# Kernel tuning notes

Hardware: AMD Instinct MI355X
Metric: run time of the kernel (lower is better)

Reference implementation:

```python
import jax, jax.numpy as jnp
import numpy as np

SCALE = 2  # scale_factor (isotropic Vec3i broadcast of init arg)
N_VOXELS = 262144
CHANNELS = 64


def setup_inputs() -> dict:
    key = jax.random.key(0)
    k1, k2 = jax.random.split(key)
    coarse_data = jax.random.normal(k1, (N_VOXELS, CHANNELS), dtype=jnp.float32)
    coarse_ijk = jax.random.randint(k2, (N_VOXELS, 3), 0, 512, dtype=jnp.int32)
    return {"coarse_data": coarse_data, "coarse_ijk": coarse_ijk}


def reference(coarse_data, coarse_ijk):
    """Nearest-neighbor subdivision of a sparse voxel grid.

    Each coarse voxel (ijk, feature) expands into SCALE**3 fine voxels at
    ijk*SCALE + offset, all carrying the parent's feature (nearest upsampling).
    Returns (fine_data [N*s^3, C], fine_ijk [N*s^3, 3]).
    """
    s = SCALE
    n_sub = s * s * s
    # offsets within each subdivided cell: [s^3, 3]
    offsets = jnp.stack(jnp.meshgrid(jnp.arange(s), jnp.arange(s), jnp.arange(s),
                                     indexing="ij"), axis=-1).reshape(-1, 3).astype(coarse_ijk.dtype)
    # fine coordinates: [N, s^3, 3] -> [N*s^3, 3]
    fine_ijk = (coarse_ijk[:, None, :] * s + offsets[None, :, :]).reshape(-1, 3)
    # nearest upsampling: repeat each coarse feature s^3 times -> [N*s^3, C]
    n, c = coarse_data.shape
    fine_data = jnp.broadcast_to(coarse_data[:, None, :], (n, n_sub, c)).reshape(-1, c)
    return fine_data, fine_ijk
```

## Files before the change

### kernel.cpp

```cpp
#include <hip/hip_runtime.h>

#define N_COARSE 262144
#define CHANNELS 64
#define DATA_F4     (N_COARSE * 8 * 16)
#define DATA_BLOCKS 131072
#define IJK_ELEMS   (N_COARSE * 8 * 3)
#define IJK_BLOCKS  24576

typedef float nfloat4 __attribute__((ext_vector_type(4)));

__global__ void __launch_bounds__(256)
upsample_fused_kernel(const nfloat4* __restrict__ in, const int* __restrict__ ijk,
                      nfloat4* __restrict__ out_data, float* __restrict__ out_ijk) {
    const int b = blockIdx.x;
    if (b < DATA_BLOCKS) {
        const size_t j   = (size_t)b * 256 + threadIdx.x;
        const size_t src = ((j >> 7) << 4) | (j & 15);
        out_data[j] = in[src];
    } else {
        const int e = (b - DATA_BLOCKS) * 256 + threadIdx.x;
        const int r = e / 3;
        const int d = e - r * 3;
        const int n = r >> 3;
        const int o = r & 7;
        const int off = (o >> (2 - d)) & 1;
        out_ijk[e] = (float)(ijk[n * 3 + d] * 2 + off);
    }
}

extern "C" void kernel_launch(void* const* d_in, const int* in_sizes, int n_in,
                              void* d_out, int out_size, void* d_ws, size_t ws_size,
                              hipStream_t stream) {
    const nfloat4* coarse_data = (const nfloat4*)d_in[0];
    const int*     coarse_ijk  = (const int*)d_in[1];

    float*   out      = (float*)d_out;
    nfloat4* out_data = (nfloat4*)out;
    float*   out_ijk  = out + (size_t)N_COARSE * 8 * CHANNELS;

    upsample_fused_kernel<<<DATA_BLOCKS + IJK_BLOCKS, 256, 0, stream>>>(
        coarse_data, coarse_ijk, out_data, out_ijk);
}
```

Measured before the change: 601.6 us.

## Use grid-stride style multi-element threads and vectorize ijk output stores

Cuts the grid from about 155k blocks to 2304 blocks, with each data thread copying 64 float4 elements and each ijk thread writing 24 float4 outputs. The ijk branch now builds four float values per thread and stores them as one 16-byte write instead of scalar 4-byte writes. The aim is to lower block launch overhead and make the ijk stores wider. The trade-off is less parallelism per element and more address arithmetic in the unrolled loops; the ijk output must also stay 16-byte aligned.

```diff
diff --git a/kernel.cpp b/kernel.cpp
--- a/kernel.cpp
+++ b/kernel.cpp
@@ -1,30 +1,46 @@
 #include <hip/hip_runtime.h>
 
-#define N_COARSE 262144
-#define CHANNELS 64
+#define N_COARSE    262144
+#define CHANNELS    64
 #define DATA_F4     (N_COARSE * 8 * 16)
-#define DATA_BLOCKS 131072
-#define IJK_ELEMS   (N_COARSE * 8 * 3)
-#define IJK_BLOCKS  24576
+#define DATA_BLOCKS 2048
+#define DATA_PER_T  64
+#define IJK_F4      ((N_COARSE * 8 * 3) / 4)
+#define IJK_BLOCKS  256
+#define IJK_PER_T   24
 
 typedef float nfloat4 __attribute__((ext_vector_type(4)));
 
 __global__ void __launch_bounds__(256)
 upsample_fused_kernel(const nfloat4* __restrict__ in, const int* __restrict__ ijk,
-                      nfloat4* __restrict__ out_data, float* __restrict__ out_ijk) {
-    const int b = blockIdx.x;
+                      nfloat4* __restrict__ out_data, nfloat4* __restrict__ out_ijk) {
+    const int b   = blockIdx.x;
+    const int tid = threadIdx.x;
     if (b < DATA_BLOCKS) {
-        const size_t j   = (size_t)b * 256 + threadIdx.x;
-        const size_t src = ((j >> 7) << 4) | (j & 15);
-        out_data[j] = in[src];
+        const size_t jbase = (size_t)b * 16384 + tid;
+        const size_t sbase = (size_t)b * 2048 + ((tid >> 7) << 4) + (tid & 15);
+#pragma unroll 8
+        for (int k = 0; k < DATA_PER_T; ++k)
+            out_data[jbase + (size_t)k * 256] = in[sbase + (size_t)k * 32];
     } else {
-        const int e = (b - DATA_BLOCKS) * 256 + threadIdx.x;
-        const int r = e / 3;
-        const int d = e - r * 3;
-        const int n = r >> 3;
-        const int o = r & 7;
-        const int off = (o >> (2 - d)) & 1;
-        out_ijk[e] = (float)(ijk[n * 3 + d] * 2 + off);
+        const int bi = b - DATA_BLOCKS;
+        const int tbase = bi * 6144 + tid;
+#pragma unroll 4
+        for (int k = 0; k < IJK_PER_T; ++k) {
+            const int t = tbase + k * 256;
+            nfloat4 v;
+#pragma unroll
+            for (int m = 0; m < 4; ++m) {
+                const int e = 4 * t + m;
+                const int r = e / 3;
+                const int d = e - r * 3;
+                const int n = r >> 3;
+                const int o = r & 7;
+                const int off = (o >> (2 - d)) & 1;
+                v[m] = (float)(ijk[n * 3 + d] * 2 + off);
+            }
+            out_ijk[t] = v;
+        }
     }
 }
 
@@ -36,7 +52,7 @@
 
     float*   out      = (float*)d_out;
     nfloat4* out_data = (nfloat4*)out;
-    float*   out_ijk  = out + (size_t)N_COARSE * 8 * CHANNELS;
+    nfloat4* out_ijk  = (nfloat4*)(out + (size_t)N_COARSE * 8 * CHANNELS);
 
     upsample_fused_kernel<<<DATA_BLOCKS + IJK_BLOCKS, 256, 0, stream>>>(
         coarse_data, coarse_ijk, out_data, out_ijk);
```

Result: no change. 610.3 us (+1.4%).
